# Performance work log

Hardware: AMD Instinct MI355X
Metric: run time of the kernel (lower is better)

The kernel has to match this reference:

```python
import jax, jax.numpy as jnp
import numpy as np

HIDDEN = 2048
NUM_HEADS = 16
KEY_DIM = 1024      # hidden * expand_k (0.5)
VALUE_DIM = 2048    # hidden * expand_v (1.0)
HEAD_K = KEY_DIM // NUM_HEADS   # 64
HEAD_V = VALUE_DIM // NUM_HEADS # 128
EPS = 1e-5
B, T = 8, 4096


def _rmsnorm(x, w, eps=EPS):
    var = jnp.mean(jnp.square(x), axis=-1, keepdims=True)
    return x * jax.lax.rsqrt(var + eps) * w


def setup_inputs() -> dict:
    key = jax.random.key(0)
    ks = jax.random.split(key, 7)
    s = 1.0 / np.sqrt(HIDDEN)
    return {
        "hidden_states": jax.random.normal(ks[0], (B, T, HIDDEN), dtype=jnp.float32),
        "recurrent_state": jax.random.normal(ks[1], (B, NUM_HEADS, HEAD_K, HEAD_V), dtype=jnp.float32),
        "norm_w": jnp.ones((HIDDEN,), dtype=jnp.float32),
        "q_w": jax.random.uniform(ks[2], (KEY_DIM, HIDDEN), jnp.float32, -s, s),
        "v_norm_w": jnp.ones((HEAD_V,), dtype=jnp.float32),
        "o_w": jax.random.uniform(ks[3], (HIDDEN, VALUE_DIM), jnp.float32, -s, s),
        "gate_w": jax.random.uniform(ks[4], (HIDDEN, HIDDEN), jnp.float32, -s, s),
    }


def reference(hidden_states, recurrent_state, norm_w, q_w, v_norm_w, o_w, gate_w):
    x = _rmsnorm(hidden_states, norm_w)                       # (B,T,D)
    q = x @ q_w.T                                             # (B,T,KEY_DIM)
    q = q.reshape(*q.shape[:2], NUM_HEADS, HEAD_K)            # (B,T,H,K)
    # L2 normalize along last dim (F.normalize default eps=1e-12 on the norm)
    norm = jnp.maximum(jnp.linalg.norm(q, axis=-1, keepdims=True), 1e-12)
    q = q / norm
    o = jnp.einsum('bthk,bhkv->bthv', q, recurrent_state)     # (B,T,H,V)
    o = _rmsnorm(o, v_norm_w)
    o = o.reshape(*o.shape[:2], VALUE_DIM)                    # (B,T,VALUE_DIM)
    o = o @ o_w.T                                             # (B,T,D)
    gate = jax.nn.sigmoid(x @ gate_w.T)                       # (B,T,D)
    return gate * o
```

## Files before the change

### kernel.cpp

```cpp
#include <hip/hip_runtime.h>

typedef unsigned short u16;
typedef unsigned int u32;
typedef __attribute__((ext_vector_type(4))) float f32x4;
typedef __attribute__((ext_vector_type(8))) short short8;
typedef __attribute__((ext_vector_type(4))) short short4v;

#define HIDDEN 2048
#define NHEADS 16
#define KEYDIM 1024
#define VALDIM 2048
#define HEADK 64
#define HEADV 128
#define NBATCH 8
#define SEQ 4096
#define NTOK (NBATCH * SEQ)

__device__ __forceinline__ u16 f2bf(float f) {
  union { float f; u32 u; } c; c.f = f;
  u32 r = c.u + 0x7FFFu + ((c.u >> 16) & 1u);
  return (u16)(r >> 16);
}
__device__ __forceinline__ float bf2f(u16 h) {
  union { u32 u; float f; } c; c.u = ((u32)h) << 16;
  return c.f;
}

__global__ __launch_bounds__(256) void cast_bf16_k(const float* __restrict__ in,
                                                   u16* __restrict__ out, int n4) {
  int i = blockIdx.x * blockDim.x + threadIdx.x;
  if (i >= n4) return;
  f32x4 v = *(const f32x4*)(in + (size_t)i * 4);
  short4v o;
  o[0] = (short)f2bf(v[0]); o[1] = (short)f2bf(v[1]);
  o[2] = (short)f2bf(v[2]); o[3] = (short)f2bf(v[3]);
  *(short4v*)(out + (size_t)i * 4) = o;
}

__global__ __launch_bounds__(256) void rmsnorm_cast_k(const float* __restrict__ x,
                                                      const float* __restrict__ w,
                                                      u16* __restrict__ xb) {
  int r = blockIdx.x;
  int tid = threadIdx.x;
  const float* xp = x + (size_t)r * HIDDEN + tid * 8;
  f32x4 v0 = *(const f32x4*)xp;
  f32x4 v1 = *(const f32x4*)(xp + 4);
  float ss = v0[0]*v0[0]+v0[1]*v0[1]+v0[2]*v0[2]+v0[3]*v0[3]
           + v1[0]*v1[0]+v1[1]*v1[1]+v1[2]*v1[2]+v1[3]*v1[3];
  #pragma unroll
  for (int m = 32; m >= 1; m >>= 1) ss += __shfl_xor(ss, m);
  __shared__ float red[4];
  if ((tid & 63) == 0) red[tid >> 6] = ss;
  __syncthreads();
  float tot = red[0] + red[1] + red[2] + red[3];
  float inv = rsqrtf(tot * (1.0f / HIDDEN) + 1e-5f);
  const float* wp = w + tid * 8;
  f32x4 w0 = *(const f32x4*)wp;
  f32x4 w1 = *(const f32x4*)(wp + 4);
  short8 o;
  o[0] = (short)f2bf(v0[0] * inv * w0[0]);
  o[1] = (short)f2bf(v0[1] * inv * w0[1]);
  o[2] = (short)f2bf(v0[2] * inv * w0[2]);
  o[3] = (short)f2bf(v0[3] * inv * w0[3]);
  o[4] = (short)f2bf(v1[0] * inv * w1[0]);
  o[5] = (short)f2bf(v1[1] * inv * w1[1]);
  o[6] = (short)f2bf(v1[2] * inv * w1[2]);
  o[7] = (short)f2bf(v1[3] * inv * w1[3]);
  *(short8*)(xb + (size_t)r * HIDDEN + tid * 8) = o;
}


__device__ __forceinline__ void gload16(const u16* g, u16* l) {
  __builtin_amdgcn_global_load_lds((const __attribute__((address_space(1))) void*)g,
                                   (__attribute__((address_space(3))) void*)l, 16, 0, 0);
}

#define BAR()                                  \
  do {                                         \
    asm volatile("" ::: "memory");             \
    __builtin_amdgcn_s_barrier();              \
    asm volatile("" ::: "memory");             \
  } while (0)

template <int MODE>
__global__ __launch_bounds__(512, 4) void gemm2b_k(const u16* __restrict__ A,
                                                   const u16* __restrict__ Bw,
                                                   void* __restrict__ Cptr,
                                                   u16* __restrict__ Aux,
                                                   int M, int N, int K) {
  extern __shared__ u16 lds[];
  const int tid = threadIdx.x;
  const int wid = tid >> 6;
  const int wm = wid >> 2;
  const int wn = wid & 3;
  const int l = tid & 63;
  const int lr = l & 15;
  const int kq = l >> 4;

  const int ntn = N >> 8;
  const int per = gridDim.x >> 3;
  const int b = blockIdx.x;
  const int sidx = (b & 7) * per + (b >> 3);
  const int mt = sidx / ntn;
  const int nt = sidx - mt * ntn;

  const u16* Ag = A + (size_t)(mt * 128) * K;
  const u16* Bg = Bw + (size_t)(nt * 256) * K;

  const int srow = tid >> 2;
  const int kel = (((tid & 3) ^ ((tid >> 3) & 3)) << 3);

#define BUFB(c) (((c) % 3) * 12288)
#define STAGE(c)                                                      \
  do {                                                                \
    const u16* _sa = Ag + (size_t)srow * K + ((c) << 5) + kel;        \
    u16* _d = lds + BUFB(c) + tid * 8;                                \
    gload16(_sa, _d);                                                 \
    const u16* _sb = Bg + (size_t)srow * K + ((c) << 5) + kel;        \
    gload16(_sb, _d + 4096);                                          \
    gload16(_sb + (size_t)128 * K, _d + 8192);                        \
  } while (0)

  int aoff[2][4], boff[4];
  #pragma unroll
  for (int mh = 0; mh < 2; ++mh) {
    #pragma unroll
    for (int mi = 0; mi < 4; ++mi) {
      int R = wm * 64 + mh * 0 + mi * 16 + lr;
      (void)R;
    }
  }
  #pragma unroll
  for (int mi = 0; mi < 4; ++mi) {
    int R = wm * 64 + mi * 16 + lr;
    aoff[0][mi] = R * 32 + ((kq ^ ((R >> 1) & 3)) << 3);
  }
  #pragma unroll
  for (int n = 0; n < 4; ++n) {
    int R = wn * 64 + n * 16 + lr;
    boff[n] = 4096 + R * 32 + ((kq ^ ((R >> 1) & 3)) << 3);
  }

  short8 afr[4], bfr[4];
  f32x4 acc[4][4] = {};

  STAGE(0);
  STAGE(1);
  asm volatile("s_waitcnt vmcnt(3)" ::: "memory");
  BAR();

  const int NT = K >> 5;
  #pragma unroll 1
  for (int c = 0; c < NT; ++c) {
    const u16* bufT = lds + BUFB(c);
    const int g2 = (c + 2 < NT);

    #pragma unroll
    for (int mi = 0; mi < 4; ++mi) afr[mi] = *(const short8*)(bufT + aoff[0][mi]);
    bfr[0] = *(const short8*)(bufT + boff[0]);
    bfr[1] = *(const short8*)(bufT + boff[1]);
    if (g2) STAGE(c + 2);
    BAR();
    __builtin_amdgcn_s_setprio(1);
    #pragma unroll
    for (int mi = 0; mi < 4; ++mi) {
      acc[mi][0] = __builtin_amdgcn_mfma_f32_16x16x32_bf16(afr[mi], bfr[0], acc[mi][0], 0, 0, 0);
      acc[mi][1] = __builtin_amdgcn_mfma_f32_16x16x32_bf16(afr[mi], bfr[1], acc[mi][1], 0, 0, 0);
    }
    __builtin_amdgcn_s_setprio(0);

    bfr[2] = *(const short8*)(bufT + boff[2]);
    bfr[3] = *(const short8*)(bufT + boff[3]);
    if (g2)              asm volatile("s_waitcnt vmcnt(3)" ::: "memory");
    else if (c + 1 < NT) asm volatile("s_waitcnt vmcnt(0)" ::: "memory");
    BAR();
    __builtin_amdgcn_s_setprio(1);
    #pragma unroll
    for (int mi = 0; mi < 4; ++mi) {
      acc[mi][2] = __builtin_amdgcn_mfma_f32_16x16x32_bf16(afr[mi], bfr[2], acc[mi][2], 0, 0, 0);
      acc[mi][3] = __builtin_amdgcn_mfma_f32_16x16x32_bf16(afr[mi], bfr[3], acc[mi][3], 0, 0, 0);
    }
    __builtin_amdgcn_s_setprio(0);
  }
#undef STAGE
#undef BUFB

  const int rowB = mt * 128 + wm * 64 + kq * 4;
  const int colB = nt * 256 + wn * 64 + lr;
  #pragma unroll
  for (int m = 0; m < 4; ++m) {
    #pragma unroll
    for (int n = 0; n < 4; ++n) {
      #pragma unroll
      for (int j = 0; j < 4; ++j) {
        int row = rowB + m * 16 + j;
        int col = colB + n * 16;
        float v = acc[m][n][j];
        if constexpr (MODE == 2) {
          size_t idx = (size_t)row * N + col;
          ((float*)Cptr)[idx] = v * bf2f(Aux[idx]);
        } else if constexpr (MODE == 4) {
          size_t idx = (size_t)row * N + col;
          float* O = (float*)Cptr;
          O[idx] = O[idx] * v;
        } else {
          if (nt < 4) {
            int h = col >> 6, k = col & 63;
            int bb = row >> 12, tok = row & (SEQ - 1);
            Aux[((size_t)(bb * NHEADS + h) * SEQ + tok) * HEADK + k] = f2bf(v);
          } else {
            int colg = col - 1024;
            float sg = 1.0f / (1.0f + __expf(-v));
            if constexpr (MODE == 5) {
              ((u16*)Cptr)[(size_t)row * HIDDEN + colg] = f2bf(sg);
            } else {
              ((float*)Cptr)[(size_t)row * HIDDEN + colg] = sg;
            }
          }
        }
      }
    }
  }
}

__global__ __launch_bounds__(256) void glaread_k(const u16* __restrict__ qT,
                                                 const float* __restrict__ S,
                                                 const float* __restrict__ vw,
                                                 u16* __restrict__ omid) {
  int bh = blockIdx.x;
  int b = bh >> 4, h = bh & 15;
  int tid = threadIdx.x;
  int w = tid >> 6, l = tid & 63;
  int lr = l & 15, kq = l >> 4;

  __shared__ u16 tile[4][16 * 136];

  const float* Sp = S + (size_t)bh * HEADK * HEADV;
  short8 bfrag[8][2];
  #pragma unroll
  for (int n = 0; n < 8; ++n) {
    #pragma unroll
    for (int s = 0; s < 2; ++s) {
      #pragma unroll
      for (int i = 0; i < 8; ++i)
        bfrag[n][s][i] =
            (short)f2bf(Sp[(size_t)(s * 32 + kq * 8 + i) * HEADV + n * 16 + lr]);
    }
  }
  float vwn[8];
  #pragma unroll
  for (int n = 0; n < 8; ++n) vwn[n] = vw[n * 16 + lr];

  const u16* qbase = qT + (size_t)bh * SEQ * HEADK;
  const int ttk = l >> 2;
  const int cc = (l & 3) * 32;

  #pragma unroll 1
  for (int it = 0; it < 8; ++it) {
    int t0 = blockIdx.y * 512 + it * 64 + w * 16;
    const u16* qp = qbase + (size_t)(t0 + lr) * HEADK;
    short8 a0 = *(const short8*)(qp + kq * 8);
    short8 a1 = *(const short8*)(qp + 32 + kq * 8);

    float ss = 0.f;
    #pragma unroll
    for (int i = 0; i < 8; ++i) {
      float x0 = bf2f((u16)a0[i]), x1 = bf2f((u16)a1[i]);
      ss += x0 * x0 + x1 * x1;
    }
    ss += __shfl_xor(ss, 16);
    ss += __shfl_xor(ss, 32);
    float sc = 1.0f / fmaxf(sqrtf(ss), 1e-12f);

    short8 an0, an1;
    #pragma unroll
    for (int i = 0; i < 8; ++i) {
      an0[i] = (short)f2bf(bf2f((u16)a0[i]) * sc);
      an1[i] = (short)f2bf(bf2f((u16)a1[i]) * sc);
    }

    f32x4 acc[8] = {};
    #pragma unroll
    for (int n = 0; n < 8; ++n) {
      acc[n] = __builtin_amdgcn_mfma_f32_16x16x32_bf16(an0, bfrag[n][0], acc[n], 0, 0, 0);
      acc[n] = __builtin_amdgcn_mfma_f32_16x16x32_bf16(an1, bfrag[n][1], acc[n], 0, 0, 0);
    }

    float part[4] = {0.f, 0.f, 0.f, 0.f};
    #pragma unroll
    for (int n = 0; n < 8; ++n) {
      #pragma unroll
      for (int j = 0; j < 4; ++j) part[j] += acc[n][j] * acc[n][j];
    }
    #pragma unroll
    for (int msk = 1; msk <= 8; msk <<= 1) {
      #pragma unroll
      for (int j = 0; j < 4; ++j) part[j] += __shfl_xor(part[j], msk);
    }
    #pragma unroll
    for (int j = 0; j < 4; ++j) {
      float inv = rsqrtf(part[j] * (1.0f / HEADV) + 1e-5f);
      #pragma unroll
      for (int n = 0; n < 8; ++n)
        tile[w][(kq * 4 + j) * 136 + n * 16 + lr] = f2bf(acc[n][j] * inv * vwn[n]);
    }
    asm volatile("s_waitcnt lgkmcnt(0)" ::: "memory");
    {
      const u16* src = &tile[w][ttk * 136 + cc];
      u16* dst = omid + (size_t)(b * SEQ + t0 + ttk) * VALDIM + h * HEADV + cc;
      short8 r0 = *(const short8*)(src);
      short8 r1 = *(const short8*)(src + 8);
      short8 r2 = *(const short8*)(src + 16);
      short8 r3 = *(const short8*)(src + 24);
      *(short8*)(dst) = r0;
      *(short8*)(dst + 8) = r1;
      *(short8*)(dst + 16) = r2;
      *(short8*)(dst + 24) = r3;
    }
    asm volatile("" ::: "memory");
  }
}

extern "C" void kernel_launch(void* const* d_in, const int* in_sizes, int n_in,
                              void* d_out, int out_size, void* d_ws, size_t ws_size,
                              hipStream_t stream) {
  const float* hs = (const float*)d_in[0];
  const float* S  = (const float*)d_in[1];
  const float* nw = (const float*)d_in[2];
  const float* qw = (const float*)d_in[3];
  const float* vw = (const float*)d_in[4];
  const float* ow = (const float*)d_in[5];
  const float* gw = (const float*)d_in[6];
  float* out = (float*)d_out;

  u16* xb   = (u16*)d_ws;
  u16* qT   = xb + (size_t)NTOK * HIDDEN;
  u16* qwb  = qT + (size_t)NTOK * KEYDIM;
  u16* gwb  = qwb + (size_t)KEYDIM * HIDDEN;
  u16* owb  = gwb + (size_t)HIDDEN * HIDDEN;
  u16* gatebuf = owb + (size_t)HIDDEN * VALDIM;
  u16* omid = xb;

  const size_t need = ((size_t)NTOK * HIDDEN * 2) * 2 + (size_t)NTOK * KEYDIM * 2 +
                      ((size_t)KEYDIM * HIDDEN + 2 * (size_t)HIDDEN * HIDDEN) * 2;
  const bool bigws = ws_size >= need;

  const size_t LDSB = 73728;

  cast_bf16_k<<<(KEYDIM * HIDDEN / 4 + 255) / 256, 256, 0, stream>>>(qw, qwb, KEYDIM * HIDDEN / 4);
  cast_bf16_k<<<(HIDDEN * HIDDEN / 4 + 255) / 256, 256, 0, stream>>>(gw, gwb, HIDDEN * HIDDEN / 4);
  cast_bf16_k<<<(HIDDEN * VALDIM / 4 + 255) / 256, 256, 0, stream>>>(ow, owb, HIDDEN * VALDIM / 4);

  rmsnorm_cast_k<<<NTOK, 256, 0, stream>>>(hs, nw, xb);

  if (bigws) {
    gemm2b_k<5><<<dim3((NTOK / 128) * ((KEYDIM + HIDDEN) / 256)), 512, LDSB, stream>>>(
        xb, qwb, gatebuf, qT, NTOK, KEYDIM + HIDDEN, HIDDEN);
  } else {
    gemm2b_k<6><<<dim3((NTOK / 128) * ((KEYDIM + HIDDEN) / 256)), 512, LDSB, stream>>>(
        xb, qwb, out, qT, NTOK, KEYDIM + HIDDEN, HIDDEN);
  }

  glaread_k<<<dim3(NBATCH * NHEADS, SEQ / 512), 256, 0, stream>>>(qT, S, vw, omid);

  if (bigws) {
    gemm2b_k<2><<<dim3((NTOK / 128) * (HIDDEN / 256)), 512, LDSB, stream>>>(
        omid, owb, out, gatebuf, NTOK, HIDDEN, VALDIM);
  } else {
    gemm2b_k<4><<<dim3((NTOK / 128) * (HIDDEN / 256)), 512, LDSB, stream>>>(
        omid, owb, out, nullptr, NTOK, HIDDEN, VALDIM);
  }
}
```

Baseline: 937.1 us.

## Enlarge GEMM tile to 256x256 and drop transposed q layout

The GEMM kernel grows its output tile from 128x256 to 256x256, doubling the A staging per stage and the accumulators per wave. It also removes one barrier per k-step and lowers the occupancy hint to 2 blocks per SM, aiming for more MFMA work per byte loaded from LDS and global memory. The q projection is now written row-major instead of head-transposed. The read kernel therefore loads q with strided rows and writes omid directly without an LDS staging tile, which trades coalescing for less shuffle work. Register pressure and LDS use (96KB) rise, and the risk is lower occupancy or spills.

```diff
diff --git a/kernel.cpp b/kernel.cpp
--- a/kernel.cpp
+++ b/kernel.cpp
@@ -83,7 +83,7 @@
   } while (0)
 
 template <int MODE>
-__global__ __launch_bounds__(512, 4) void gemm2b_k(const u16* __restrict__ A,
+__global__ __launch_bounds__(512, 2) void gemm1t_k(const u16* __restrict__ A,
                                                    const u16* __restrict__ Bw,
                                                    void* __restrict__ Cptr,
                                                    u16* __restrict__ Aux,
@@ -104,21 +104,22 @@
   const int mt = sidx / ntn;
   const int nt = sidx - mt * ntn;
 
-  const u16* Ag = A + (size_t)(mt * 128) * K;
+  const u16* Ag = A + (size_t)(mt * 256) * K;
   const u16* Bg = Bw + (size_t)(nt * 256) * K;
 
   const int srow = tid >> 2;
   const int kel = (((tid & 3) ^ ((tid >> 3) & 3)) << 3);
 
-#define BUFB(c) (((c) % 3) * 12288)
+#define BUFB(c) (((c) % 3) << 14)
 #define STAGE(c)                                                      \
   do {                                                                \
     const u16* _sa = Ag + (size_t)srow * K + ((c) << 5) + kel;        \
     u16* _d = lds + BUFB(c) + tid * 8;                                \
     gload16(_sa, _d);                                                 \
+    gload16(_sa + (size_t)128 * K, _d + 4096);                        \
     const u16* _sb = Bg + (size_t)srow * K + ((c) << 5) + kel;        \
-    gload16(_sb, _d + 4096);                                          \
-    gload16(_sb + (size_t)128 * K, _d + 8192);                        \
+    gload16(_sb, _d + 8192);                                          \
+    gload16(_sb + (size_t)128 * K, _d + 12288);                       \
   } while (0)
 
   int aoff[2][4], boff[4];
@@ -126,69 +127,72 @@
   for (int mh = 0; mh < 2; ++mh) {
     #pragma unroll
     for (int mi = 0; mi < 4; ++mi) {
-      int R = wm * 64 + mh * 0 + mi * 16 + lr;
-      (void)R;
-    }
-  }
-  #pragma unroll
-  for (int mi = 0; mi < 4; ++mi) {
-    int R = wm * 64 + mi * 16 + lr;
-    aoff[0][mi] = R * 32 + ((kq ^ ((R >> 1) & 3)) << 3);
+      int R = wm * 128 + mh * 64 + mi * 16 + lr;
+      aoff[mh][mi] = R * 32 + ((kq ^ ((R >> 1) & 3)) << 3);
+    }
   }
   #pragma unroll
   for (int n = 0; n < 4; ++n) {
     int R = wn * 64 + n * 16 + lr;
-    boff[n] = 4096 + R * 32 + ((kq ^ ((R >> 1) & 3)) << 3);
+    boff[n] = 8192 + R * 32 + ((kq ^ ((R >> 1) & 3)) << 3);
   }
 
   short8 afr[4], bfr[4];
-  f32x4 acc[4][4] = {};
+  f32x4 acc[8][4] = {};
 
   STAGE(0);
   STAGE(1);
-  asm volatile("s_waitcnt vmcnt(3)" ::: "memory");
+  asm volatile("s_waitcnt vmcnt(4)" ::: "memory");
   BAR();
 
   const int NT = K >> 5;
   #pragma unroll 1
   for (int c = 0; c < NT; ++c) {
     const u16* bufT = lds + BUFB(c);
-    const int g2 = (c + 2 < NT);
-
+
+    #pragma unroll
+    for (int n = 0; n < 4; ++n) bfr[n] = *(const short8*)(bufT + boff[n]);
     #pragma unroll
     for (int mi = 0; mi < 4; ++mi) afr[mi] = *(const short8*)(bufT + aoff[0][mi]);
-    bfr[0] = *(const short8*)(bufT + boff[0]);
-    bfr[1] = *(const short8*)(bufT + boff[1]);
-    if (g2) STAGE(c + 2);
-    BAR();
+
+    if (c + 2 < NT) STAGE(c + 2);
+
     __builtin_amdgcn_s_setprio(1);
     #pragma unroll
     for (int mi = 0; mi < 4; ++mi) {
-      acc[mi][0] = __builtin_amdgcn_mfma_f32_16x16x32_bf16(afr[mi], bfr[0], acc[mi][0], 0, 0, 0);
-      acc[mi][1] = __builtin_amdgcn_mfma_f32_16x16x32_bf16(afr[mi], bfr[1], acc[mi][1], 0, 0, 0);
+      #pragma unroll
+      for (int n = 0; n < 4; ++n)
+        acc[mi][n] = __builtin_amdgcn_mfma_f32_16x16x32_bf16(afr[mi], bfr[n], acc[mi][n], 0, 0, 0);
     }
     __builtin_amdgcn_s_setprio(0);
 
-    bfr[2] = *(const short8*)(bufT + boff[2]);
-    bfr[3] = *(const short8*)(bufT + boff[3]);
-    if (g2)              asm volatile("s_waitcnt vmcnt(3)" ::: "memory");
-    else if (c + 1 < NT) asm volatile("s_waitcnt vmcnt(0)" ::: "memory");
-    BAR();
+    #pragma unroll
+    for (int mi = 0; mi < 4; ++mi) afr[mi] = *(const short8*)(bufT + aoff[1][mi]);
+
     __builtin_amdgcn_s_setprio(1);
     #pragma unroll
     for (int mi = 0; mi < 4; ++mi) {
-      acc[mi][2] = __builtin_amdgcn_mfma_f32_16x16x32_bf16(afr[mi], bfr[2], acc[mi][2], 0, 0, 0);
-      acc[mi][3] = __builtin_amdgcn_mfma_f32_16x16x32_bf16(afr[mi], bfr[3], acc[mi][3], 0, 0, 0);
+      #pragma unroll
+      for (int n = 0; n < 4; ++n)
+        acc[4 + mi][n] = __builtin_amdgcn_mfma_f32_16x16x32_bf16(afr[mi], bfr[n], acc[4 + mi][n], 0, 0, 0);
     }
     __builtin_amdgcn_s_setprio(0);
+
+    if (c + 2 < NT) {
+      asm volatile("s_waitcnt vmcnt(4)" ::: "memory");
+      BAR();
+    } else if (c + 1 < NT) {
+      asm volatile("s_waitcnt vmcnt(0)" ::: "memory");
+      BAR();
+    }
   }
 #undef STAGE
 #undef BUFB
 
-  const int rowB = mt * 128 + wm * 64 + kq * 4;
+  const int rowB = mt * 256 + wm * 128 + kq * 4;
   const int colB = nt * 256 + wn * 64 + lr;
   #pragma unroll
-  for (int m = 0; m < 4; ++m) {
+  for (int m = 0; m < 8; ++m) {
     #pragma unroll
     for (int n = 0; n < 4; ++n) {
       #pragma unroll
@@ -205,9 +209,7 @@
           O[idx] = O[idx] * v;
         } else {
           if (nt < 4) {
-            int h = col >> 6, k = col & 63;
-            int bb = row >> 12, tok = row & (SEQ - 1);
-            Aux[((size_t)(bb * NHEADS + h) * SEQ + tok) * HEADK + k] = f2bf(v);
+            Aux[(size_t)row * KEYDIM + col] = f2bf(v);
           } else {
             int colg = col - 1024;
             float sg = 1.0f / (1.0f + __expf(-v));
@@ -223,7 +225,7 @@
   }
 }
 
-__global__ __launch_bounds__(256) void glaread_k(const u16* __restrict__ qT,
+__global__ __launch_bounds__(256) void glaread_k(const u16* __restrict__ q,
                                                  const float* __restrict__ S,
                                                  const float* __restrict__ vw,
                                                  u16* __restrict__ omid) {
@@ -233,8 +235,6 @@
   int w = tid >> 6, l = tid & 63;
   int lr = l & 15, kq = l >> 4;
 
-  __shared__ u16 tile[4][16 * 136];
-
   const float* Sp = S + (size_t)bh * HEADK * HEADV;
   short8 bfrag[8][2];
   #pragma unroll
@@ -251,14 +251,10 @@
   #pragma unroll
   for (int n = 0; n < 8; ++n) vwn[n] = vw[n * 16 + lr];
 
-  const u16* qbase = qT + (size_t)bh * SEQ * HEADK;
-  const int ttk = l >> 2;
-  const int cc = (l & 3) * 32;
-
   #pragma unroll 1
-  for (int it = 0; it < 8; ++it) {
-    int t0 = blockIdx.y * 512 + it * 64 + w * 16;
-    const u16* qp = qbase + (size_t)(t0 + lr) * HEADK;
+  for (int it = 0; it < 4; ++it) {
+    int t0 = blockIdx.y * 256 + it * 64 + w * 16;
+    const u16* qp = q + (size_t)(b * SEQ + t0 + lr) * KEYDIM + h * HEADK;
     short8 a0 = *(const short8*)(qp + kq * 8);
     short8 a1 = *(const short8*)(qp + 32 + kq * 8);
 
@@ -300,24 +296,12 @@
     #pragma unroll
     for (int j = 0; j < 4; ++j) {
       float inv = rsqrtf(part[j] * (1.0f / HEADV) + 1e-5f);
+      int tok = t0 + kq * 4 + j;
+      u16* op = omid + (size_t)(b * SEQ + tok) * VALDIM + h * HEADV;
       #pragma unroll
       for (int n = 0; n < 8; ++n)
-        tile[w][(kq * 4 + j) * 136 + n * 16 + lr] = f2bf(acc[n][j] * inv * vwn[n]);
-    }
-    asm volatile("s_waitcnt lgkmcnt(0)" ::: "memory");
-    {
-      const u16* src = &tile[w][ttk * 136 + cc];
-      u16* dst = omid + (size_t)(b * SEQ + t0 + ttk) * VALDIM + h * HEADV + cc;
-      short8 r0 = *(const short8*)(src);
-      short8 r1 = *(const short8*)(src + 8);
-      short8 r2 = *(const short8*)(src + 16);
-      short8 r3 = *(const short8*)(src + 24);
-      *(short8*)(dst) = r0;
-      *(short8*)(dst + 8) = r1;
-      *(short8*)(dst + 16) = r2;
-      *(short8*)(dst + 24) = r3;
-    }
-    asm volatile("" ::: "memory");
+        op[n * 16 + lr] = f2bf(acc[n][j] * inv * vwn[n]);
+    }
   }
 }
 
@@ -334,8 +318,8 @@
   float* out = (float*)d_out;
 
   u16* xb   = (u16*)d_ws;
-  u16* qT   = xb + (size_t)NTOK * HIDDEN;
-  u16* qwb  = qT + (size_t)NTOK * KEYDIM;
+  u16* q    = xb + (size_t)NTOK * HIDDEN;
+  u16* qwb  = q + (size_t)NTOK * KEYDIM;
   u16* gwb  = qwb + (size_t)KEYDIM * HIDDEN;
   u16* owb  = gwb + (size_t)HIDDEN * HIDDEN;
   u16* gatebuf = owb + (size_t)HIDDEN * VALDIM;
@@ -345,7 +329,7 @@
                       ((size_t)KEYDIM * HIDDEN + 2 * (size_t)HIDDEN * HIDDEN) * 2;
   const bool bigws = ws_size >= need;
 
-  const size_t LDSB = 73728;
+  const size_t LDSB = 98304;
 
   cast_bf16_k<<<(KEYDIM * HIDDEN / 4 + 255) / 256, 256, 0, stream>>>(qw, qwb, KEYDIM * HIDDEN / 4);
   cast_bf16_k<<<(HIDDEN * HIDDEN / 4 + 255) / 256, 256, 0, stream>>>(gw, gwb, HIDDEN * HIDDEN / 4);
@@ -354,20 +338,20 @@
   rmsnorm_cast_k<<<NTOK, 256, 0, stream>>>(hs, nw, xb);
 
   if (bigws) {
-    gemm2b_k<5><<<dim3((NTOK / 128) * ((KEYDIM + HIDDEN) / 256)), 512, LDSB, stream>>>(
-        xb, qwb, gatebuf, qT, NTOK, KEYDIM + HIDDEN, HIDDEN);
+    gemm1t_k<5><<<dim3((NTOK / 256) * ((KEYDIM + HIDDEN) / 256)), 512, LDSB, stream>>>(
+        xb, qwb, gatebuf, q, NTOK, KEYDIM + HIDDEN, HIDDEN);
   } else {
-    gemm2b_k<6><<<dim3((NTOK / 128) * ((KEYDIM + HIDDEN) / 256)), 512, LDSB, stream>>>(
-        xb, qwb, out, qT, NTOK, KEYDIM + HIDDEN, HIDDEN);
-  }
-
-  glaread_k<<<dim3(NBATCH * NHEADS, SEQ / 512), 256, 0, stream>>>(qT, S, vw, omid);
+    gemm1t_k<6><<<dim3((NTOK / 256) * ((KEYDIM + HIDDEN) / 256)), 512, LDSB, stream>>>(
+        xb, qwb, out, q, NTOK, KEYDIM + HIDDEN, HIDDEN);
+  }
+
+  glaread_k<<<dim3(NBATCH * NHEADS, SEQ / 256), 256, 0, stream>>>(q, S, vw, omid);
 
   if (bigws) {
-    gemm2b_k<2><<<dim3((NTOK / 128) * (HIDDEN / 256)), 512, LDSB, stream>>>(
+    gemm1t_k<2><<<dim3((NTOK / 256) * (HIDDEN / 256)), 512, LDSB, stream>>>(
         omid, owb, out, gatebuf, NTOK, HIDDEN, VALDIM);
   } else {
-    gemm2b_k<4><<<dim3((NTOK / 128) * (HIDDEN / 256)), 512, LDSB, stream>>>(
+    gemm1t_k<4><<<dim3((NTOK / 256) * (HIDDEN / 256)), 512, LDSB, stream>>>(
         omid, owb, out, nullptr, NTOK, HIDDEN, VALDIM);
   }
 }
```

Result: faster. 885.4 us (-5.5%).
